# Kernel tuning notes

Measured on AMD Instinct MI355X. Metric: run time of the kernel, lower is better.

## Reference

```python
import jax, jax.numpy as jnp
import numpy as np

# Production shapes from the module docstring: cs (B,90,512), cs_p (B,90,256,256), mask (B,256,256)
B, H, LP, W, L = 16, 90, 512, 256, 256
K = 384  # number of valid (non-NaN) columns in cs == number of positive mask pixels per item


def setup_inputs() -> dict:
    key = jax.random.key(0)
    k1, k2, k3 = jax.random.split(key, 3)
    cs = jax.random.normal(k1, (B, H, LP), dtype=jnp.float32)
    # NaN padding after the first K columns (same pattern in every row, as the
    # original's reshape([height, -1]) requires equal valid counts per row)
    cs = jnp.where(jnp.arange(LP) < K, cs, jnp.nan)
    cs_p = jax.random.normal(k2, (B, H, W, L), dtype=jnp.float32)
    # exactly K positive overpass pixels per item, at random flat positions
    perm = jax.vmap(lambda k: jax.random.permutation(k, W * L))(jax.random.split(k3, B))
    mask = jnp.zeros((B, W * L), dtype=jnp.int32)
    mask = mask.at[jnp.arange(B)[:, None], perm[:, :K]].set(1)
    return {"cs": cs, "cs_p": cs_p, "overpass_mask": mask.reshape(B, W, L)}


def _per_item_mse(cs_i, cs_p_i, mask_i):
    # cs_i: (H, LP) with NaN padding; valid columns identical across rows, so
    # torch's cs_i[~isnan(cs_i)].reshape(H, -1) == gather of the K valid columns
    # in ascending column order (stable argsort of the NaN flag, False first).
    cols = jnp.argsort(jnp.isnan(cs_i[0]), stable=True)[:K]            # (K,)
    cs_sel = cs_i[:, cols]                                             # (H, K)
    # torch's cs_p_i[mask.expand(H,-1,-1)].reshape(H, -1): per height-row,
    # masked pixels in row-major (w, l) order -> flat-index gather.
    pos = jnp.argsort(mask_i.reshape(-1) <= 0, stable=True)[:K]        # (K,)
    cs_p_sel = cs_p_i.reshape(cs_p_i.shape[0], -1)[:, pos]             # (H, K)
    return jnp.mean((cs_sel - cs_p_sel) ** 2)


def reference(cs, cs_p, overpass_mask):
    # per-item mean MSE, then mean over batch (matches torch.stack(...).mean())
    return jnp.mean(jax.vmap(_per_item_mse)(cs, cs_p, overpass_mask))
```

## Files before the change

### kernel.cpp

```cpp
#include <hip/hip_runtime.h>

#define B_     16
#define H_     90
#define LP_    512
#define WL_    65536
#define K_     384
#define BHK    (B_ * H_ * K_)
#define HG     3
#define NH     (H_ / HG)

__global__ __launch_bounds__(1024) void select_kernel(const int* __restrict__ mask,
                                                      int* __restrict__ pos,
                                                      float* __restrict__ out) {
    const int b = blockIdx.x;
    const int t = threadIdx.x;
    if (b == 0 && t == 0) out[0] = 0.0f;
    const int lane = t & 63, wid = t >> 6;

    __shared__ int ws[16][16];
    unsigned long long fl = 0ull;
    int wexcl[16];

    const int4* __restrict__ src = (const int4*)(mask + (size_t)b * WL_);
    #pragma unroll
    for (int i = 0; i < 16; ++i) {
        const int4 v = src[i * 1024 + t];
        const int f0 = v.x != 0, f1 = v.y != 0, f2 = v.z != 0, f3 = v.w != 0;
        fl |= (unsigned long long)(f0 | (f1 << 1) | (f2 << 2) | (f3 << 3)) << (i * 4);
        const int c = f0 + f1 + f2 + f3;
        int incl = c;
        #pragma unroll
        for (int d = 1; d < 64; d <<= 1) {
            const int x = __shfl_up(incl, d, 64);
            if (lane >= d) incl += x;
        }
        if (lane == 63) ws[i][wid] = incl;
        wexcl[i] = incl - c;
    }
    __syncthreads();

    int* __restrict__ pb = pos + b * K_;
    int running = 0;
    #pragma unroll
    for (int i = 0; i < 16; ++i) {
        int wbase = 0, tot = 0;
        #pragma unroll
        for (int w = 0; w < 16; ++w) {
            const int x = ws[i][w];
            tot += x;
            if (w < wid) wbase += x;
        }
        int wp = running + wbase + wexcl[i];
        running += tot;
        const int gb = i * 4096 + t * 4;
        if ((fl >> (i * 4 + 0)) & 1) pb[wp++] = gb + 0;
        if ((fl >> (i * 4 + 1)) & 1) pb[wp++] = gb + 1;
        if ((fl >> (i * 4 + 2)) & 1) pb[wp++] = gb + 2;
        if ((fl >> (i * 4 + 3)) & 1) pb[wp]   = gb + 3;
    }
}

__global__ __launch_bounds__(384) void mse_kernel(const float* __restrict__ cs,
                                                  const float* __restrict__ csp,
                                                  const int* __restrict__ pos,
                                                  float* __restrict__ out) {
    const int g  = blockIdx.x;
    const int b  = g / NH;
    const int h0 = (g - b * NH) * HG;
    const int k  = threadIdx.x;
    const int p  = pos[b * K_ + k];
    const size_t r0 = (size_t)(b * H_ + h0);
    float acc = 0.0f;
    #pragma unroll
    for (int j = 0; j < HG; ++j) {
        const float a = cs [(r0 + j) * LP_ + k];
        const float c = csp[(r0 + j) * WL_ + p];
        const float d = a - c;
        acc = fmaf(d, d, acc);
    }
    #pragma unroll
    for (int off = 32; off > 0; off >>= 1) acc += __shfl_down(acc, off, 64);
    __shared__ float s[6];
    const int lane = k & 63, wid = k >> 6;
    if (lane == 0) s[wid] = acc;
    __syncthreads();
    if (k == 0) {
        const float sum = s[0] + s[1] + s[2] + s[3] + s[4] + s[5];
        atomicAdd(out, sum * (1.0f / (float)BHK));
    }
}

extern "C" void kernel_launch(void* const* d_in, const int* in_sizes, int n_in,
                              void* d_out, int out_size, void* d_ws, size_t ws_size,
                              hipStream_t stream) {
    const float* cs   = (const float*)d_in[0];
    const float* csp  = (const float*)d_in[1];
    const int*   mask = (const int*)d_in[2];
    float* out = (float*)d_out;

    int* pos = (int*)d_ws;

    select_kernel<<<B_,      1024, 0, stream>>>(mask, pos, out);
    mse_kernel   <<<B_ * NH,  384, 0, stream>>>(cs, csp, pos, out);
}
```

Before: 444.1 us.

## Replace scattered pixel gather with dense streaming pass over masked tensor

The selection kernel now writes a per-pixel rank map (a short per pixel, -1 when unmasked) instead of a compact list of positions. The MSE kernel streams every pixel of cs_p with coalesced float4 loads across all 90 height rows and only accumulates where the rank is non-negative, looking up the matching cs column by rank. This trades scattered, latency-bound gathers for reading the whole tensor, far more bytes, at full bandwidth.

```diff
diff --git a/kernel.cpp b/kernel.cpp
--- a/kernel.cpp
+++ b/kernel.cpp
@@ -6,11 +6,11 @@
 #define WL_    65536
 #define K_     384
 #define BHK    (B_ * H_ * K_)
-#define HG     3
-#define NH     (H_ / HG)
+#define NCH    64
+#define CELEM  1024
 
 __global__ __launch_bounds__(1024) void select_kernel(const int* __restrict__ mask,
-                                                      int* __restrict__ pos,
+                                                      short* __restrict__ rank,
                                                       float* __restrict__ out) {
     const int b = blockIdx.x;
     const int t = threadIdx.x;
@@ -39,7 +39,7 @@
     }
     __syncthreads();
 
-    int* __restrict__ pb = pos + b * K_;
+    short* __restrict__ rb = rank + (size_t)b * WL_;
     int running = 0;
     #pragma unroll
     for (int i = 0; i < 16; ++i) {
@@ -50,42 +50,61 @@
             tot += x;
             if (w < wid) wbase += x;
         }
-        int wp = running + wbase + wexcl[i];
+        const int f0 = (int)(fl >> (i * 4 + 0)) & 1;
+        const int f1 = (int)(fl >> (i * 4 + 1)) & 1;
+        const int f2 = (int)(fl >> (i * 4 + 2)) & 1;
+        const int f3 = (int)(fl >> (i * 4 + 3)) & 1;
+        const int w0 = running + wbase + wexcl[i];
+        const int w1 = w0 + f0, w2 = w1 + f1, w3 = w2 + f2;
         running += tot;
-        const int gb = i * 4096 + t * 4;
-        if ((fl >> (i * 4 + 0)) & 1) pb[wp++] = gb + 0;
-        if ((fl >> (i * 4 + 1)) & 1) pb[wp++] = gb + 1;
-        if ((fl >> (i * 4 + 2)) & 1) pb[wp++] = gb + 2;
-        if ((fl >> (i * 4 + 3)) & 1) pb[wp]   = gb + 3;
+        short4 o;
+        o.x = f0 ? (short)w0 : (short)-1;
+        o.y = f1 ? (short)w1 : (short)-1;
+        o.z = f2 ? (short)w2 : (short)-1;
+        o.w = f3 ? (short)w3 : (short)-1;
+        *(short4*)(rb + i * 4096 + t * 4) = o;
     }
 }
 
-__global__ __launch_bounds__(384) void mse_kernel(const float* __restrict__ cs,
+__global__ __launch_bounds__(256) void mse_stream(const float* __restrict__ cs,
                                                   const float* __restrict__ csp,
-                                                  const int* __restrict__ pos,
+                                                  const short* __restrict__ rank,
                                                   float* __restrict__ out) {
-    const int g  = blockIdx.x;
-    const int b  = g / NH;
-    const int h0 = (g - b * NH) * HG;
-    const int k  = threadIdx.x;
-    const int p  = pos[b * K_ + k];
-    const size_t r0 = (size_t)(b * H_ + h0);
-    float acc = 0.0f;
+    const int blk = blockIdx.x;
+    const int b = blk >> 6;
+    const int c = blk & (NCH - 1);
+    const int t = threadIdx.x;
+    const int e0 = c * CELEM + t * 4;
+
+    const short4 r4 = *(const short4*)(rank + (size_t)b * WL_ + e0);
+    const float* __restrict__ cspb = csp + ((size_t)b * H_) * WL_ + e0;
+    const float* __restrict__ csb  = cs  + ((size_t)b * H_) * LP_;
+
+    float acc0 = 0.0f, acc1 = 0.0f;
+    #pragma unroll 2
+    for (int h = 0; h < H_; h += 2) {
+        const float4 va = *(const float4*)(cspb + (size_t)h * WL_);
+        const float4 vb = *(const float4*)(cspb + (size_t)(h + 1) * WL_);
+        const float* __restrict__ ca = csb + h * LP_;
+        const float* __restrict__ cb = ca + LP_;
+        if (r4.x >= 0) { float d0 = ca[r4.x] - va.x, d1 = cb[r4.x] - vb.x;
+                         acc0 = fmaf(d0, d0, acc0); acc1 = fmaf(d1, d1, acc1); }
+        if (r4.y >= 0) { float d0 = ca[r4.y] - va.y, d1 = cb[r4.y] - vb.y;
+                         acc0 = fmaf(d0, d0, acc0); acc1 = fmaf(d1, d1, acc1); }
+        if (r4.z >= 0) { float d0 = ca[r4.z] - va.z, d1 = cb[r4.z] - vb.z;
+                         acc0 = fmaf(d0, d0, acc0); acc1 = fmaf(d1, d1, acc1); }
+        if (r4.w >= 0) { float d0 = ca[r4.w] - va.w, d1 = cb[r4.w] - vb.w;
+                         acc0 = fmaf(d0, d0, acc0); acc1 = fmaf(d1, d1, acc1); }
+    }
+    float v = acc0 + acc1;
     #pragma unroll
-    for (int j = 0; j < HG; ++j) {
-        const float a = cs [(r0 + j) * LP_ + k];
-        const float c = csp[(r0 + j) * WL_ + p];
-        const float d = a - c;
-        acc = fmaf(d, d, acc);
-    }
-    #pragma unroll
-    for (int off = 32; off > 0; off >>= 1) acc += __shfl_down(acc, off, 64);
-    __shared__ float s[6];
-    const int lane = k & 63, wid = k >> 6;
-    if (lane == 0) s[wid] = acc;
+    for (int off = 32; off > 0; off >>= 1) v += __shfl_down(v, off, 64);
+    __shared__ float s[4];
+    const int lane = t & 63, wid = t >> 6;
+    if (lane == 0) s[wid] = v;
     __syncthreads();
-    if (k == 0) {
-        const float sum = s[0] + s[1] + s[2] + s[3] + s[4] + s[5];
+    if (t == 0) {
+        const float sum = s[0] + s[1] + s[2] + s[3];
         atomicAdd(out, sum * (1.0f / (float)BHK));
     }
 }
@@ -98,8 +117,8 @@
     const int*   mask = (const int*)d_in[2];
     float* out = (float*)d_out;
 
-    int* pos = (int*)d_ws;
+    short* rank = (short*)d_ws;
 
-    select_kernel<<<B_,      1024, 0, stream>>>(mask, pos, out);
-    mse_kernel   <<<B_ * NH,  384, 0, stream>>>(cs, csp, pos, out);
+    select_kernel<<<B_,        1024, 0, stream>>>(mask, rank, out);
+    mse_stream   <<<B_ * NCH,   256, 0, stream>>>(cs, csp, rank, out);
 }
```

Result: slower. 539.3 us (+21.4%).

## Split mask compaction into chunked count and scatter kernels across many blocks

Applied to the files above, without the earlier changes.

The single-block-per-item stream compaction is replaced by a two-pass scheme. A count kernel computes per-1024-element chunk counts over 1024 blocks, then a scatter kernel scans the chunk counts and writes positions. The aim is to spread the 4 MB mask read over far more CUs than the previous 16 blocks allowed. The cost is an extra kernel launch and reading the mask twice.

```diff
diff --git a/kernel.cpp b/kernel.cpp
--- a/kernel.cpp
+++ b/kernel.cpp
@@ -6,58 +6,74 @@
 #define WL_    65536
 #define K_     384
 #define BHK    (B_ * H_ * K_)
+#define CHUNK  1024
+#define NCHUNK (WL_ / CHUNK)
+#define NBLK   (B_ * NCHUNK)
 #define HG     3
 #define NH     (H_ / HG)
 
-__global__ __launch_bounds__(1024) void select_kernel(const int* __restrict__ mask,
-                                                      int* __restrict__ pos,
-                                                      float* __restrict__ out) {
-    const int b = blockIdx.x;
+__global__ __launch_bounds__(256) void count_kernel(const int* __restrict__ mask,
+                                                    int* __restrict__ cnt,
+                                                    float* __restrict__ out) {
+    if (blockIdx.x == 0 && threadIdx.x == 0) out[0] = 0.0f;
+    const int4 v = ((const int4*)(mask + (size_t)blockIdx.x * CHUNK))[threadIdx.x];
+    int c = (v.x != 0) + (v.y != 0) + (v.z != 0) + (v.w != 0);
+    #pragma unroll
+    for (int off = 32; off > 0; off >>= 1) c += __shfl_down(c, off, 64);
+    __shared__ int s[4];
+    const int lane = threadIdx.x & 63, wid = threadIdx.x >> 6;
+    if (lane == 0) s[wid] = c;
+    __syncthreads();
+    if (threadIdx.x == 0) cnt[blockIdx.x] = s[0] + s[1] + s[2] + s[3];
+}
+
+__global__ __launch_bounds__(256) void scatter_kernel(const int* __restrict__ mask,
+                                                      const int* __restrict__ cnt,
+                                                      int* __restrict__ pos) {
+    const int blk = blockIdx.x;
+    const int b = blk >> 6;
+    const int j = blk & (NCHUNK - 1);
     const int t = threadIdx.x;
-    if (b == 0 && t == 0) out[0] = 0.0f;
+    const int4 v = ((const int4*)(mask + (size_t)blk * CHUNK))[t];
+    const int f0 = v.x != 0, f1 = v.y != 0, f2 = v.z != 0, f3 = v.w != 0;
+    const int c = f0 + f1 + f2 + f3;
     const int lane = t & 63, wid = t >> 6;
 
-    __shared__ int ws[16][16];
-    unsigned long long fl = 0ull;
-    int wexcl[16];
+    __shared__ int ws[4];
+    __shared__ int sOff;
 
-    const int4* __restrict__ src = (const int4*)(mask + (size_t)b * WL_);
+    int incl = c;
     #pragma unroll
-    for (int i = 0; i < 16; ++i) {
-        const int4 v = src[i * 1024 + t];
-        const int f0 = v.x != 0, f1 = v.y != 0, f2 = v.z != 0, f3 = v.w != 0;
-        fl |= (unsigned long long)(f0 | (f1 << 1) | (f2 << 2) | (f3 << 3)) << (i * 4);
-        const int c = f0 + f1 + f2 + f3;
-        int incl = c;
+    for (int d = 1; d < 64; d <<= 1) {
+        const int x = __shfl_up(incl, d, 64);
+        if (lane >= d) incl += x;
+    }
+    if (lane == 63) ws[wid] = incl;
+
+    if (wid == 0) {
+        const int cc = cnt[(b << 6) + lane];
+        int ci = cc;
         #pragma unroll
         for (int d = 1; d < 64; d <<= 1) {
-            const int x = __shfl_up(incl, d, 64);
-            if (lane >= d) incl += x;
+            const int x = __shfl_up(ci, d, 64);
+            if (lane >= d) ci += x;
         }
-        if (lane == 63) ws[i][wid] = incl;
-        wexcl[i] = incl - c;
+        if (lane == j) sOff = ci - cc;
     }
     __syncthreads();
 
-    int* __restrict__ pb = pos + b * K_;
-    int running = 0;
+    int wbase = 0;
     #pragma unroll
-    for (int i = 0; i < 16; ++i) {
-        int wbase = 0, tot = 0;
-        #pragma unroll
-        for (int w = 0; w < 16; ++w) {
-            const int x = ws[i][w];
-            tot += x;
-            if (w < wid) wbase += x;
-        }
-        int wp = running + wbase + wexcl[i];
-        running += tot;
-        const int gb = i * 4096 + t * 4;
-        if ((fl >> (i * 4 + 0)) & 1) pb[wp++] = gb + 0;
-        if ((fl >> (i * 4 + 1)) & 1) pb[wp++] = gb + 1;
-        if ((fl >> (i * 4 + 2)) & 1) pb[wp++] = gb + 2;
-        if ((fl >> (i * 4 + 3)) & 1) pb[wp]   = gb + 3;
-    }
+    for (int wi = 0; wi < 4; ++wi) if (wi < wid) wbase += ws[wi];
+    const int excl = wbase + incl - c;
+
+    const int gbase = j * CHUNK + t * 4;
+    int w = sOff + excl;
+    int* __restrict__ p = pos + b * K_;
+    if (f0) p[w++] = gbase + 0;
+    if (f1) p[w++] = gbase + 1;
+    if (f2) p[w++] = gbase + 2;
+    if (f3) p[w]   = gbase + 3;
 }
 
 __global__ __launch_bounds__(384) void mse_kernel(const float* __restrict__ cs,
@@ -72,9 +88,9 @@
     const size_t r0 = (size_t)(b * H_ + h0);
     float acc = 0.0f;
     #pragma unroll
-    for (int j = 0; j < HG; ++j) {
-        const float a = cs [(r0 + j) * LP_ + k];
-        const float c = csp[(r0 + j) * WL_ + p];
+    for (int jj = 0; jj < HG; ++jj) {
+        const float a = cs [(r0 + jj) * LP_ + k];
+        const float c = csp[(r0 + jj) * WL_ + p];
         const float d = a - c;
         acc = fmaf(d, d, acc);
     }
@@ -99,7 +115,9 @@
     float* out = (float*)d_out;
 
     int* pos = (int*)d_ws;
+    int* cnt = pos + B_ * K_;
 
-    select_kernel<<<B_,      1024, 0, stream>>>(mask, pos, out);
-    mse_kernel   <<<B_ * NH,  384, 0, stream>>>(cs, csp, pos, out);
+    count_kernel  <<<NBLK,    256, 0, stream>>>(mask, cnt, out);
+    scatter_kernel<<<NBLK,    256, 0, stream>>>(mask, cnt, pos);
+    mse_kernel    <<<B_ * NH, 384, 0, stream>>>(cs, csp, pos, out);
 }
```

Measured after the change: 431.5 us. -2.8%, faster.
